# Optimization experiments

Hardware: AMD Instinct MI355X
Metric: run time of the kernel (lower is better)

The kernel has to match this reference:

```python
import jax, jax.numpy as jnp
import numpy as np

N, E, D, H, Z = 100000, 1600000, 128, 256, 64


def _gconv(x, src, dst, W, b, n):
    # DGL GraphConv, norm='both': D_in^{-1/2} A D_out^{-1/2} x W + b
    ones = jnp.ones(src.shape, x.dtype)
    deg_out = jnp.clip(jax.ops.segment_sum(ones, src, num_segments=n), 1.0)
    deg_in = jnp.clip(jax.ops.segment_sum(ones, dst, num_segments=n), 1.0)
    h = x * (deg_out ** -0.5)[:, None]          # scale by src out-degree
    agg = jax.ops.segment_sum(h[src], dst, num_segments=n)  # SpMM gather/scatter
    return (agg * (deg_in ** -0.5)[:, None]) @ W + b


def setup_inputs() -> dict:
    key = jax.random.key(0)
    ks = jax.random.split(key, 8)
    return {
        "features": jax.random.normal(ks[0], (N, D), jnp.float32),
        "src": jax.random.randint(ks[1], (E,), 0, N, jnp.int32),
        "dst": jax.random.randint(ks[2], (E,), 0, N, jnp.int32),
        "eps": jax.random.normal(ks[3], (N, Z), jnp.float32),
        "W1": jax.random.normal(ks[4], (D, H), jnp.float32) * (1.0 / np.sqrt(D)),
        "b1": jnp.zeros((H,), jnp.float32),
        "W2": jax.random.normal(ks[5], (H, 2 * Z), jnp.float32) * (1.0 / np.sqrt(H)),
        "b2": jnp.zeros((2 * Z,), jnp.float32),
        "W3": jax.random.normal(ks[6], (Z, D), jnp.float32) * (1.0 / np.sqrt(Z)),
        "b3": jnp.zeros((D,), jnp.float32),
    }


def reference(features, src, dst, eps, W1, b1, W2, b2, W3, b3):
    n = features.shape[0]
    h = jax.nn.relu(_gconv(features, src, dst, W1, b1, n))
    mean_logvar = _gconv(h, src, dst, W2, b2, n)
    mean, log_var = jnp.split(mean_logvar, 2, axis=1)
    z = eps * jnp.exp(0.5 * log_var) + mean  # reparameterization
    recon = _gconv(z, src, dst, W3, b3, n)
    return recon, mean, log_var
```

## Files before the change

### kernel.cpp

```cpp
#include <hip/hip_runtime.h>
#include <math.h>


#define MAXD 64
#define FBSH 8
#define EPT  16

typedef short short8 __attribute__((ext_vector_type(8)));
typedef float f32x4 __attribute__((ext_vector_type(4)));

__device__ __forceinline__ unsigned short f2bf(float f) {
  union { float f; unsigned u; } c; c.f = f;
  unsigned r = c.u + 0x7FFF + ((c.u >> 16) & 1);
  return (unsigned short)(r >> 16);
}
__device__ __forceinline__ float bf2f(unsigned short b) {
  return __builtin_bit_cast(float, (unsigned)b << 16);
}

__global__ __launch_bounds__(256) void k_bucket2(const int* __restrict__ src,
    const int* __restrict__ dst, int* __restrict__ bcd, int* __restrict__ bcs,
    int* __restrict__ bktd, unsigned char* __restrict__ srec,
    int E, int NFB, int cap2) {
  extern __shared__ int sh[];
  int* lcd = sh;
  int* lbd = sh + NFB;
  int* lcs = sh + 2 * NFB;
  int* lbs = sh + 3 * NFB;
  int tid = threadIdx.x;
  for (int i = tid; i < 4 * NFB; i += 256) sh[i] = 0;
  __syncthreads();
  int e0 = blockIdx.x * (256 * EPT);
  #pragma unroll 4
  for (int j = 0; j < EPT; j++) {
    int e = e0 + j * 256 + tid;
    if (e < E) {
      int d = dst[e]; atomicAdd(&lcd[d >> FBSH], 1);
      int s = src[e]; atomicAdd(&lcs[s >> FBSH], 1);
    }
  }
  __syncthreads();
  for (int fb = tid; fb < NFB; fb += 256) {
    int c = lcd[fb];
    if (c) lbd[fb] = atomicAdd(&bcd[fb], c);
    int cs = lcs[fb];
    if (cs) lbs[fb] = atomicAdd(&bcs[fb], cs);
  }
  __syncthreads();
  #pragma unroll 4
  for (int j = 0; j < EPT; j++) {
    int e = e0 + j * 256 + tid;
    if (e < E) {
      int d = dst[e]; int s = src[e];
      int fbd = d >> FBSH;
      int od = atomicAdd(&lbd[fbd], 1);
      if (od < cap2) bktd[(size_t)fbd * cap2 + od] = ((d & 255) << 24) | s;
      int fbs = s >> FBSH;
      int os = atomicAdd(&lbs[fbs], 1);
      if (os < cap2) srec[(size_t)fbs * cap2 + os] = (unsigned char)(s & 255);
    }
  }
}

__global__ __launch_bounds__(256) void k_csr(const int* __restrict__ bktd,
    const int* __restrict__ bcd, int* __restrict__ cnt, int* __restrict__ ebuf,
    int N, int cap2) {
  __shared__ int lcnt[256];
  int fb = blockIdx.x;
  int tid = threadIdx.x;
  lcnt[tid] = 0;
  __syncthreads();
  int m = bcd[fb]; m = m < cap2 ? m : cap2;
  const int* rec = bktd + (size_t)fb * cap2;
  for (int i0 = tid * 4; i0 < m; i0 += 1024) {
    if (i0 + 4 <= m) {
      int4 r = *(const int4*)(rec + i0);
      int dl, s, p;
      dl = (unsigned)r.x >> 24; s = r.x & 0xFFFFFF;
      p = atomicAdd(&lcnt[dl], 1);
      if (p < MAXD) ebuf[((size_t)(fb << FBSH) + dl) * MAXD + p] = s;
      dl = (unsigned)r.y >> 24; s = r.y & 0xFFFFFF;
      p = atomicAdd(&lcnt[dl], 1);
      if (p < MAXD) ebuf[((size_t)(fb << FBSH) + dl) * MAXD + p] = s;
      dl = (unsigned)r.z >> 24; s = r.z & 0xFFFFFF;
      p = atomicAdd(&lcnt[dl], 1);
      if (p < MAXD) ebuf[((size_t)(fb << FBSH) + dl) * MAXD + p] = s;
      dl = (unsigned)r.w >> 24; s = r.w & 0xFFFFFF;
      p = atomicAdd(&lcnt[dl], 1);
      if (p < MAXD) ebuf[((size_t)(fb << FBSH) + dl) * MAXD + p] = s;
    } else {
      for (int k = i0; k < m; k++) {
        int r = rec[k];
        int dl = (unsigned)r >> 24; int s = r & 0xFFFFFF;
        int p = atomicAdd(&lcnt[dl], 1);
        if (p < MAXD) ebuf[((size_t)(fb << FBSH) + dl) * MAXD + p] = s;
      }
    }
  }
  __syncthreads();
  int node = (fb << FBSH) + tid;
  if (node < N) cnt[node] = lcnt[tid];
}

__global__ __launch_bounds__(256) void k_deg(const unsigned char* __restrict__ srec,
    const int* __restrict__ bcs, int* __restrict__ degout, int N, int cap2) {
  __shared__ int lh[256];
  int fb = blockIdx.x;
  int tid = threadIdx.x;
  lh[tid] = 0;
  __syncthreads();
  int m = bcs[fb]; m = m < cap2 ? m : cap2;
  const unsigned char* rec = srec + (size_t)fb * cap2;
  for (int i0 = tid * 4; i0 < m; i0 += 1024) {
    if (i0 + 4 <= m) {
      uchar4 r = *(const uchar4*)(rec + i0);
      atomicAdd(&lh[r.x], 1); atomicAdd(&lh[r.y], 1);
      atomicAdd(&lh[r.z], 1); atomicAdd(&lh[r.w], 1);
    } else {
      for (int k = i0; k < m; k++) atomicAdd(&lh[rec[k]], 1);
    }
  }
  __syncthreads();
  int node = (fb << FBSH) + tid;
  if (node < N) degout[node] = lh[tid];
}

__global__ __launch_bounds__(256) void k_scale(const int* __restrict__ degout,
    const int* __restrict__ cnt, float* __restrict__ sout,
    float* __restrict__ sin_, int N) {
  int i = blockIdx.x * 256 + threadIdx.x;
  if (i >= N) return;
  int dO = degout[i]; if (dO < 1) dO = 1;
  int dI = cnt[i];    if (dI < 1) dI = 1;
  sout[i] = rsqrtf((float)dO);
  sin_[i] = rsqrtf((float)dI);
}

__global__ __launch_bounds__(256) void k_cvt(const float* __restrict__ in,
    unsigned short* __restrict__ out, int n) {
  int i = (blockIdx.x * 256 + threadIdx.x) * 4;
  if (i >= n) return;
  float4 f = *(const float4*)(in + i);
  unsigned lo = (unsigned)f2bf(f.x) | ((unsigned)f2bf(f.y) << 16);
  unsigned hi = (unsigned)f2bf(f.z) | ((unsigned)f2bf(f.w) << 16);
  uint2 o; o.x = lo; o.y = hi;
  *(uint2*)(out + i) = o;
}

template <int K, int OC>
__global__ __launch_bounds__(256) void k_wrepack(const float* __restrict__ W,
    short* __restrict__ Wp) {
  constexpr int KC = K / 32;
  constexpr int TOT = (OC / 16) * KC * 64;
  int t = blockIdx.x * 256 + threadIdx.x;
  if (t >= TOT) return;
  int lane = t & 63;
  int kc = (t >> 6) % KC;
  int nt = t / (KC * 64);
  int n = nt * 16 + (lane & 15);
  int k0 = kc * 32 + ((lane >> 4) * 8);
  short8 v;
  #pragma unroll
  for (int j = 0; j < 8; j++) v[j] = (short)f2bf(W[(size_t)(k0 + j) * OC + n]);
  *(short8*)(Wp + (size_t)t * 8) = v;
}

template <int K, int OC, bool RELU, bool BIAS, bool OUTBF16>
__global__ __launch_bounds__(256) void k_gemm_mfma(
    const unsigned short* __restrict__ A, const short* __restrict__ Wp,
    const float* __restrict__ bias, void* __restrict__ Cout, int N) {
  constexpr int KC = K / 32;
  constexpr int NT = OC / 16;
  int lane = threadIdx.x & 63;
  int wv = threadIdx.x >> 6;
  int m0 = (blockIdx.x * 4 + wv) * 16;
  if (m0 >= N) return;
  int mrow = m0 + (lane & 15);
  if (mrow >= N) mrow = N - 1;
  int q = lane >> 4;
  short8 av[KC];
  #pragma unroll
  for (int kc = 0; kc < KC; kc++)
    av[kc] = *(const short8*)(A + (size_t)mrow * K + kc * 32 + q * 8);
  int col0 = lane & 15;
  int rbase = m0 + q * 4;
  #pragma unroll
  for (int nt = 0; nt < NT; nt++) {
    f32x4 acc = {0.f, 0.f, 0.f, 0.f};
    #pragma unroll
    for (int kc = 0; kc < KC; kc++) {
      short8 bv = *(const short8*)(Wp + ((size_t)(nt * KC + kc) * 64 + lane) * 8);
      acc = __builtin_amdgcn_mfma_f32_16x16x32_bf16(av[kc], bv, acc, 0, 0, 0);
    }
    int col = nt * 16 + col0;
    float bb = BIAS ? bias[col] : 0.f;
    #pragma unroll
    for (int r = 0; r < 4; r++) {
      int row = rbase + r;
      if (row < N) {
        float v = acc[r] + bb;
        if (RELU) v = fmaxf(v, 0.f);
        if (OUTBF16) ((unsigned short*)Cout)[(size_t)row * OC + col] = f2bf(v);
        else         ((float*)Cout)[(size_t)row * OC + col] = v;
      }
    }
  }
}

__global__ __launch_bounds__(256) void k_spmm128b(const unsigned short* __restrict__ x,
    const int* __restrict__ ebuf, const int* __restrict__ cnt,
    const float* __restrict__ sout, const float* __restrict__ sin_,
    unsigned short* __restrict__ out, int N) {
  int lane = threadIdx.x & 63;
  int v = blockIdx.x * 4 + (threadIdx.x >> 6);
  if (v >= N) return;
  v = __builtin_amdgcn_readfirstlane(v);
  int c = cnt[v]; c = c < MAXD ? c : MAXD;
  const int* el = ebuf + (size_t)v * MAXD;
  int u_l = 0; float w_l = 0.f;
  if (lane < c) { u_l = el[lane]; w_l = sout[u_l]; }
  float ax = 0.f, ay = 0.f;
  int i = 0;
  for (; i + 4 <= c; i += 4) {
    #pragma unroll
    for (int j = 0; j < 4; j++) {
      int u = __shfl(u_l, i + j);
      float w = __shfl(w_l, i + j);
      unsigned p = *(const unsigned*)(x + (size_t)u * 128 + lane * 2);
      float lo = __builtin_bit_cast(float, p << 16);
      float hi = __builtin_bit_cast(float, p & 0xFFFF0000u);
      ax = fmaf(w, lo, ax); ay = fmaf(w, hi, ay);
    }
  }
  for (; i < c; i++) {
    int u = __shfl(u_l, i);
    float w = __shfl(w_l, i);
    unsigned p = *(const unsigned*)(x + (size_t)u * 128 + lane * 2);
    float lo = __builtin_bit_cast(float, p << 16);
    float hi = __builtin_bit_cast(float, p & 0xFFFF0000u);
    ax = fmaf(w, lo, ax); ay = fmaf(w, hi, ay);
  }
  float sv = sin_[v];
  unsigned o = (unsigned)f2bf(sv * ax) | ((unsigned)f2bf(sv * ay) << 16);
  *(unsigned*)(out + (size_t)v * 128 + lane * 2) = o;
}

__global__ __launch_bounds__(256) void k_spmm2b(const unsigned short* __restrict__ hw,
    const int* __restrict__ ebuf, const int* __restrict__ cnt,
    const float* __restrict__ sout, const float* __restrict__ sin_,
    const float* __restrict__ b2, const float* __restrict__ eps,
    float* __restrict__ mean_out, float* __restrict__ logvar_out,
    unsigned short* __restrict__ z, int N) {
  int lane = threadIdx.x & 63;
  int v = blockIdx.x * 4 + (threadIdx.x >> 6);
  if (v >= N) return;
  v = __builtin_amdgcn_readfirstlane(v);
  int c = cnt[v]; c = c < MAXD ? c : MAXD;
  const int* el = ebuf + (size_t)v * MAXD;
  int u_l = 0; float w_l = 0.f;
  if (lane < c) { u_l = el[lane]; w_l = sout[u_l]; }
  float ax = 0.f, ay = 0.f;
  int i = 0;
  for (; i + 4 <= c; i += 4) {
    #pragma unroll
    for (int j = 0; j < 4; j++) {
      int u = __shfl(u_l, i + j);
      float w = __shfl(w_l, i + j);
      unsigned p = *(const unsigned*)(hw + (size_t)u * 128 + lane * 2);
      float lo = __builtin_bit_cast(float, p << 16);
      float hi = __builtin_bit_cast(float, p & 0xFFFF0000u);
      ax = fmaf(w, lo, ax); ay = fmaf(w, hi, ay);
    }
  }
  for (; i < c; i++) {
    int u = __shfl(u_l, i);
    float w = __shfl(w_l, i);
    unsigned p = *(const unsigned*)(hw + (size_t)u * 128 + lane * 2);
    float lo = __builtin_bit_cast(float, p << 16);
    float hi = __builtin_bit_cast(float, p & 0xFFFF0000u);
    ax = fmaf(w, lo, ax); ay = fmaf(w, hi, ay);
  }
  float sv = sin_[v];
  float2 bb = ((const float2*)b2)[lane];
  float mx = fmaf(sv, ax, bb.x);
  float my = fmaf(sv, ay, bb.y);
  if (lane < 32) ((float2*)mean_out)[(size_t)v * 32 + lane] = make_float2(mx, my);
  else           ((float2*)logvar_out)[(size_t)v * 32 + (lane - 32)] = make_float2(mx, my);
  float lx = __shfl(mx, (lane & 31) + 32);
  float ly = __shfl(my, (lane & 31) + 32);
  if (lane < 32) {
    float2 e2 = ((const float2*)eps)[(size_t)v * 32 + lane];
    float zx = fmaf(e2.x, expf(0.5f * lx), mx);
    float zy = fmaf(e2.y, expf(0.5f * ly), my);
    unsigned o = (unsigned)f2bf(zx) | ((unsigned)f2bf(zy) << 16);
    *(unsigned*)(z + (size_t)v * 64 + lane * 2) = o;
  }
}

__global__ __launch_bounds__(256) void k_spmm64b(const unsigned short* __restrict__ z,
    const int* __restrict__ ebuf, const int* __restrict__ cnt,
    const float* __restrict__ sout, const float* __restrict__ sin_,
    unsigned short* __restrict__ aggz, int N) {
  int lane = threadIdx.x & 63;
  int v = blockIdx.x * 4 + (threadIdx.x >> 6);
  if (v >= N) return;
  v = __builtin_amdgcn_readfirstlane(v);
  int c = cnt[v]; c = c < MAXD ? c : MAXD;
  const int* el = ebuf + (size_t)v * MAXD;
  int u_l = 0; float w_l = 0.f;
  if (lane < c) { u_l = el[lane]; w_l = sout[u_l]; }
  float a = 0.f;
  int i = 0;
  for (; i + 8 <= c; i += 8) {
    #pragma unroll
    for (int j = 0; j < 8; j++) {
      int u = __shfl(u_l, i + j);
      float w = __shfl(w_l, i + j);
      a = fmaf(w, bf2f(z[(size_t)u * 64 + lane]), a);
    }
  }
  for (; i < c; i++) {
    int u = __shfl(u_l, i);
    float w = __shfl(w_l, i);
    a = fmaf(w, bf2f(z[(size_t)u * 64 + lane]), a);
  }
  aggz[(size_t)v * 64 + lane] = f2bf(sin_[v] * a);
}

extern "C" void kernel_launch(void* const* d_in, const int* in_sizes, int n_in,
                              void* d_out, int out_size, void* d_ws, size_t ws_size,
                              hipStream_t stream) {
  const float* features = (const float*)d_in[0];
  const int*   src      = (const int*)d_in[1];
  const int*   dst      = (const int*)d_in[2];
  const float* eps      = (const float*)d_in[3];
  const float* W1       = (const float*)d_in[4];
  const float* b1       = (const float*)d_in[5];
  const float* W2       = (const float*)d_in[6];
  const float* b2       = (const float*)d_in[7];
  const float* W3       = (const float*)d_in[8];
  const float* b3       = (const float*)d_in[9];
  const int E = in_sizes[1];
  const int N = in_sizes[3] / 64;
  float* out = (float*)d_out;

  const int NFB = (N + 255) >> FBSH;
  const int cap2 = ((E / NFB) + 2048 + 255) & ~255;

  char* ws = (char*)d_ws;
  int* degout = (int*)ws;            ws += (size_t)N * 4;
  int* cnt    = (int*)ws;            ws += (size_t)N * 4;
  int* bcd    = (int*)ws;            ws += (size_t)NFB * 4;
  int* bcs    = (int*)ws;            ws += (size_t)NFB * 4;
  int* ebuf   = (int*)ws;            ws += (size_t)N * MAXD * 4;
  float* sout = (float*)ws;          ws += (size_t)N * 4;
  float* sin_ = (float*)ws;          ws += (size_t)N * 4;
  short* W1p  = (short*)ws;          ws += 128 * 256 * 2;
  short* W2p  = (short*)ws;          ws += 256 * 128 * 2;
  short* W3p  = (short*)ws;          ws += 64 * 128 * 2;
  char* R1    = ws;                  ws += (size_t)N * 256;
  char* R2    = ws;                  ws += (size_t)N * 256;

  unsigned short* xb    = (unsigned short*)R1;
  unsigned short* hwb   = (unsigned short*)R1;
  unsigned short* aggzb = (unsigned short*)R1;
  unsigned short* agg1b = (unsigned short*)R2;
  unsigned short* zb    = (unsigned short*)R2;
  int* bktd = (int*)R2;
  unsigned char* srec = (unsigned char*)(R2 + (size_t)NFB * cap2 * 4);

  unsigned short* h     = (unsigned short*)out;
  float* recon          = out;
  float* mean_out       = out + (size_t)N * 128;
  float* logvar_out     = out + (size_t)N * 192;

  hipMemsetAsync(degout, 0, (size_t)N * 8 + (size_t)NFB * 8, stream);

  const size_t shA = (size_t)4 * NFB * 4;
  k_bucket2<<<(E + 256 * EPT - 1) / (256 * EPT), 256, shA, stream>>>(
      src, dst, bcd, bcs, bktd, srec, E, NFB, cap2);
  k_csr<<<NFB, 256, 0, stream>>>(bktd, bcd, cnt, ebuf, N, cap2);
  k_deg<<<NFB, 256, 0, stream>>>(srec, bcs, degout, N, cap2);
  k_scale<<<(N + 255) / 256, 256, 0, stream>>>(degout, cnt, sout, sin_, N);
  k_cvt<<<((N * 128 / 4) + 255) / 256, 256, 0, stream>>>(features, xb, N * 128);
  k_wrepack<128, 256><<<16, 256, 0, stream>>>(W1, W1p);
  k_wrepack<256, 128><<<16, 256, 0, stream>>>(W2, W2p);
  k_wrepack<64, 128><<<4, 256, 0, stream>>>(W3, W3p);

  k_spmm128b<<<(N + 3) / 4, 256, 0, stream>>>(xb, ebuf, cnt, sout, sin_, agg1b, N);
  k_gemm_mfma<128, 256, true, true, true>
      <<<(N + 63) / 64, 256, 0, stream>>>(agg1b, W1p, b1, h, N);

  k_gemm_mfma<256, 128, false, false, true>
      <<<(N + 63) / 64, 256, 0, stream>>>(h, W2p, nullptr, hwb, N);
  k_spmm2b<<<(N + 3) / 4, 256, 0, stream>>>(hwb, ebuf, cnt, sout, sin_, b2, eps,
                                            mean_out, logvar_out, zb, N);

  k_spmm64b<<<(N + 3) / 4, 256, 0, stream>>>(zb, ebuf, cnt, sout, sin_, aggzb, N);
  k_gemm_mfma<64, 128, false, true, false>
      <<<(N + 63) / 64, 256, 0, stream>>>(aggzb, W3p, b3, recon, N);
}
```

Baseline: 541.2 us.

## Pre-scale rows by source-degree norm and vectorize SpMM gathers to 16-byte loads

```diff
diff --git a/kernel.cpp b/kernel.cpp
--- a/kernel.cpp
+++ b/kernel.cpp
@@ -63,8 +63,8 @@
 }
 
 __global__ __launch_bounds__(256) void k_csr(const int* __restrict__ bktd,
-    const int* __restrict__ bcd, int* __restrict__ cnt, int* __restrict__ ebuf,
-    int N, int cap2) {
+    const int* __restrict__ bcd, int* __restrict__ cnt, float* __restrict__ sin_,
+    int* __restrict__ ebuf, int N, int cap2) {
   __shared__ int lcnt[256];
   int fb = blockIdx.x;
   int tid = threadIdx.x;
@@ -99,11 +99,15 @@
   }
   __syncthreads();
   int node = (fb << FBSH) + tid;
-  if (node < N) cnt[node] = lcnt[tid];
+  if (node < N) {
+    int c = lcnt[tid];
+    cnt[node] = c;
+    sin_[node] = rsqrtf((float)(c < 1 ? 1 : c));
+  }
 }
 
 __global__ __launch_bounds__(256) void k_deg(const unsigned char* __restrict__ srec,
-    const int* __restrict__ bcs, int* __restrict__ degout, int N, int cap2) {
+    const int* __restrict__ bcs, float* __restrict__ sout, int N, int cap2) {
   __shared__ int lh[256];
   int fb = blockIdx.x;
   int tid = threadIdx.x;
@@ -122,27 +126,20 @@
   }
   __syncthreads();
   int node = (fb << FBSH) + tid;
-  if (node < N) degout[node] = lh[tid];
-}
-
-__global__ __launch_bounds__(256) void k_scale(const int* __restrict__ degout,
-    const int* __restrict__ cnt, float* __restrict__ sout,
-    float* __restrict__ sin_, int N) {
-  int i = blockIdx.x * 256 + threadIdx.x;
-  if (i >= N) return;
-  int dO = degout[i]; if (dO < 1) dO = 1;
-  int dI = cnt[i];    if (dI < 1) dI = 1;
-  sout[i] = rsqrtf((float)dO);
-  sin_[i] = rsqrtf((float)dI);
+  if (node < N) {
+    int d = lh[tid];
+    sout[node] = rsqrtf((float)(d < 1 ? 1 : d));
+  }
 }
 
 __global__ __launch_bounds__(256) void k_cvt(const float* __restrict__ in,
-    unsigned short* __restrict__ out, int n) {
+    const float* __restrict__ sout, unsigned short* __restrict__ out, int n) {
   int i = (blockIdx.x * 256 + threadIdx.x) * 4;
   if (i >= n) return;
+  float s = sout[i >> 7];
   float4 f = *(const float4*)(in + i);
-  unsigned lo = (unsigned)f2bf(f.x) | ((unsigned)f2bf(f.y) << 16);
-  unsigned hi = (unsigned)f2bf(f.z) | ((unsigned)f2bf(f.w) << 16);
+  unsigned lo = (unsigned)f2bf(s * f.x) | ((unsigned)f2bf(s * f.y) << 16);
+  unsigned hi = (unsigned)f2bf(s * f.z) | ((unsigned)f2bf(s * f.w) << 16);
   uint2 o; o.x = lo; o.y = hi;
   *(uint2*)(out + i) = o;
 }
@@ -165,10 +162,11 @@
   *(short8*)(Wp + (size_t)t * 8) = v;
 }
 
-template <int K, int OC, bool RELU, bool BIAS, bool OUTBF16>
+template <int K, int OC, bool RELU, bool BIAS, bool OUTBF16, bool SOUT>
 __global__ __launch_bounds__(256) void k_gemm_mfma(
     const unsigned short* __restrict__ A, const short* __restrict__ Wp,
-    const float* __restrict__ bias, void* __restrict__ Cout, int N) {
+    const float* __restrict__ bias, const float* __restrict__ srow,
+    void* __restrict__ Cout, int N) {
   constexpr int KC = K / 32;
   constexpr int NT = OC / 16;
   int lane = threadIdx.x & 63;
@@ -184,6 +182,14 @@
     av[kc] = *(const short8*)(A + (size_t)mrow * K + kc * 32 + q * 8);
   int col0 = lane & 15;
   int rbase = m0 + q * 4;
+  float sr[4];
+  if (SOUT) {
+    #pragma unroll
+    for (int r = 0; r < 4; r++) {
+      int row = rbase + r;
+      sr[r] = (row < N) ? srow[row] : 1.f;
+    }
+  }
   #pragma unroll
   for (int nt = 0; nt < NT; nt++) {
     f32x4 acc = {0.f, 0.f, 0.f, 0.f};
@@ -200,6 +206,7 @@
       if (row < N) {
         float v = acc[r] + bb;
         if (RELU) v = fmaxf(v, 0.f);
+        if (SOUT) v *= sr[r];
         if (OUTBF16) ((unsigned short*)Cout)[(size_t)row * OC + col] = f2bf(v);
         else         ((float*)Cout)[(size_t)row * OC + col] = v;
       }
@@ -207,45 +214,73 @@
   }
 }
 
-__global__ __launch_bounds__(256) void k_spmm128b(const unsigned short* __restrict__ x,
+__global__ __launch_bounds__(256) void k_spmm128v(const unsigned short* __restrict__ x,
     const int* __restrict__ ebuf, const int* __restrict__ cnt,
-    const float* __restrict__ sout, const float* __restrict__ sin_,
-    unsigned short* __restrict__ out, int N) {
+    const float* __restrict__ sin_, unsigned short* __restrict__ out, int N) {
   int lane = threadIdx.x & 63;
   int v = blockIdx.x * 4 + (threadIdx.x >> 6);
   if (v >= N) return;
   v = __builtin_amdgcn_readfirstlane(v);
   int c = cnt[v]; c = c < MAXD ? c : MAXD;
   const int* el = ebuf + (size_t)v * MAXD;
-  int u_l = 0; float w_l = 0.f;
-  if (lane < c) { u_l = el[lane]; w_l = sout[u_l]; }
-  float ax = 0.f, ay = 0.f;
+  int u_l = (lane < c) ? el[lane] : 0;
+  int q = lane >> 4;
+  int fo = (lane & 15) * 8;
+  float a[8] = {0, 0, 0, 0, 0, 0, 0, 0};
   int i = 0;
-  for (; i + 4 <= c; i += 4) {
-    #pragma unroll
-    for (int j = 0; j < 4; j++) {
-      int u = __shfl(u_l, i + j);
-      float w = __shfl(w_l, i + j);
-      unsigned p = *(const unsigned*)(x + (size_t)u * 128 + lane * 2);
-      float lo = __builtin_bit_cast(float, p << 16);
-      float hi = __builtin_bit_cast(float, p & 0xFFFF0000u);
-      ax = fmaf(w, lo, ax); ay = fmaf(w, hi, ay);
-    }
-  }
-  for (; i < c; i++) {
-    int u = __shfl(u_l, i);
-    float w = __shfl(w_l, i);
-    unsigned p = *(const unsigned*)(x + (size_t)u * 128 + lane * 2);
-    float lo = __builtin_bit_cast(float, p << 16);
-    float hi = __builtin_bit_cast(float, p & 0xFFFF0000u);
-    ax = fmaf(w, lo, ax); ay = fmaf(w, hi, ay);
-  }
-  float sv = sin_[v];
-  unsigned o = (unsigned)f2bf(sv * ax) | ((unsigned)f2bf(sv * ay) << 16);
-  *(unsigned*)(out + (size_t)v * 128 + lane * 2) = o;
-}
-
-__global__ __launch_bounds__(256) void k_spmm2b(const unsigned short* __restrict__ hw,
+  for (; i + 8 <= c; i += 8) {
+    int u0 = __shfl(u_l, i + q);
+    int u1 = __shfl(u_l, i + 4 + q);
+    uint4 p0 = *(const uint4*)(x + (size_t)u0 * 128 + fo);
+    uint4 p1 = *(const uint4*)(x + (size_t)u1 * 128 + fo);
+    a[0] += __builtin_bit_cast(float, p0.x << 16);
+    a[1] += __builtin_bit_cast(float, p0.x & 0xFFFF0000u);
+    a[2] += __builtin_bit_cast(float, p0.y << 16);
+    a[3] += __builtin_bit_cast(float, p0.y & 0xFFFF0000u);
+    a[4] += __builtin_bit_cast(float, p0.z << 16);
+    a[5] += __builtin_bit_cast(float, p0.z & 0xFFFF0000u);
+    a[6] += __builtin_bit_cast(float, p0.w << 16);
+    a[7] += __builtin_bit_cast(float, p0.w & 0xFFFF0000u);
+    a[0] += __builtin_bit_cast(float, p1.x << 16);
+    a[1] += __builtin_bit_cast(float, p1.x & 0xFFFF0000u);
+    a[2] += __builtin_bit_cast(float, p1.y << 16);
+    a[3] += __builtin_bit_cast(float, p1.y & 0xFFFF0000u);
+    a[4] += __builtin_bit_cast(float, p1.z << 16);
+    a[5] += __builtin_bit_cast(float, p1.z & 0xFFFF0000u);
+    a[6] += __builtin_bit_cast(float, p1.w << 16);
+    a[7] += __builtin_bit_cast(float, p1.w & 0xFFFF0000u);
+  }
+  for (; i < c; i += 4) {
+    int eidx = i + q;
+    int u = __shfl(u_l, eidx);
+    uint4 p = *(const uint4*)(x + (size_t)u * 128 + fo);
+    if (eidx >= c) { p.x = 0; p.y = 0; p.z = 0; p.w = 0; }
+    a[0] += __builtin_bit_cast(float, p.x << 16);
+    a[1] += __builtin_bit_cast(float, p.x & 0xFFFF0000u);
+    a[2] += __builtin_bit_cast(float, p.y << 16);
+    a[3] += __builtin_bit_cast(float, p.y & 0xFFFF0000u);
+    a[4] += __builtin_bit_cast(float, p.z << 16);
+    a[5] += __builtin_bit_cast(float, p.z & 0xFFFF0000u);
+    a[6] += __builtin_bit_cast(float, p.w << 16);
+    a[7] += __builtin_bit_cast(float, p.w & 0xFFFF0000u);
+  }
+  #pragma unroll
+  for (int j = 0; j < 8; j++) {
+    a[j] += __shfl_xor(a[j], 16);
+    a[j] += __shfl_xor(a[j], 32);
+  }
+  if (lane < 16) {
+    float sv = sin_[v];
+    uint4 o;
+    o.x = (unsigned)f2bf(sv * a[0]) | ((unsigned)f2bf(sv * a[1]) << 16);
+    o.y = (unsigned)f2bf(sv * a[2]) | ((unsigned)f2bf(sv * a[3]) << 16);
+    o.z = (unsigned)f2bf(sv * a[4]) | ((unsigned)f2bf(sv * a[5]) << 16);
+    o.w = (unsigned)f2bf(sv * a[6]) | ((unsigned)f2bf(sv * a[7]) << 16);
+    *(uint4*)(out + (size_t)v * 128 + fo) = o;
+  }
+}
+
+__global__ __launch_bounds__(256) void k_spmm2v(const unsigned short* __restrict__ hw,
     const int* __restrict__ ebuf, const int* __restrict__ cnt,
     const float* __restrict__ sout, const float* __restrict__ sin_,
     const float* __restrict__ b2, const float* __restrict__ eps,
@@ -257,74 +292,151 @@
   v = __builtin_amdgcn_readfirstlane(v);
   int c = cnt[v]; c = c < MAXD ? c : MAXD;
   const int* el = ebuf + (size_t)v * MAXD;
-  int u_l = 0; float w_l = 0.f;
-  if (lane < c) { u_l = el[lane]; w_l = sout[u_l]; }
-  float ax = 0.f, ay = 0.f;
+  int u_l = (lane < c) ? el[lane] : 0;
+  int q = lane >> 4;
+  int fo = (lane & 15) * 8;
+  float a[8] = {0, 0, 0, 0, 0, 0, 0, 0};
   int i = 0;
-  for (; i + 4 <= c; i += 4) {
-    #pragma unroll
-    for (int j = 0; j < 4; j++) {
-      int u = __shfl(u_l, i + j);
-      float w = __shfl(w_l, i + j);
-      unsigned p = *(const unsigned*)(hw + (size_t)u * 128 + lane * 2);
-      float lo = __builtin_bit_cast(float, p << 16);
-      float hi = __builtin_bit_cast(float, p & 0xFFFF0000u);
-      ax = fmaf(w, lo, ax); ay = fmaf(w, hi, ay);
-    }
-  }
-  for (; i < c; i++) {
-    int u = __shfl(u_l, i);
-    float w = __shfl(w_l, i);
-    unsigned p = *(const unsigned*)(hw + (size_t)u * 128 + lane * 2);
-    float lo = __builtin_bit_cast(float, p << 16);
-    float hi = __builtin_bit_cast(float, p & 0xFFFF0000u);
-    ax = fmaf(w, lo, ax); ay = fmaf(w, hi, ay);
+  for (; i + 8 <= c; i += 8) {
+    int u0 = __shfl(u_l, i + q);
+    int u1 = __shfl(u_l, i + 4 + q);
+    uint4 p0 = *(const uint4*)(hw + (size_t)u0 * 128 + fo);
+    uint4 p1 = *(const uint4*)(hw + (size_t)u1 * 128 + fo);
+    a[0] += __builtin_bit_cast(float, p0.x << 16);
+    a[1] += __builtin_bit_cast(float, p0.x & 0xFFFF0000u);
+    a[2] += __builtin_bit_cast(float, p0.y << 16);
+    a[3] += __builtin_bit_cast(float, p0.y & 0xFFFF0000u);
+    a[4] += __builtin_bit_cast(float, p0.z << 16);
+    a[5] += __builtin_bit_cast(float, p0.z & 0xFFFF0000u);
+    a[6] += __builtin_bit_cast(float, p0.w << 16);
+    a[7] += __builtin_bit_cast(float, p0.w & 0xFFFF0000u);
+    a[0] += __builtin_bit_cast(float, p1.x << 16);
+    a[1] += __builtin_bit_cast(float, p1.x & 0xFFFF0000u);
+    a[2] += __builtin_bit_cast(float, p1.y << 16);
+    a[3] += __builtin_bit_cast(float, p1.y & 0xFFFF0000u);
+    a[4] += __builtin_bit_cast(float, p1.z << 16);
+    a[5] += __builtin_bit_cast(float, p1.z & 0xFFFF0000u);
+    a[6] += __builtin_bit_cast(float, p1.w << 16);
+    a[7] += __builtin_bit_cast(float, p1.w & 0xFFFF0000u);
+  }
+  for (; i < c; i += 4) {
+    int eidx = i + q;
+    int u = __shfl(u_l, eidx);
+    uint4 p = *(const uint4*)(hw + (size_t)u * 128 + fo);
+    if (eidx >= c) { p.x = 0; p.y = 0; p.z = 0; p.w = 0; }
+    a[0] += __builtin_bit_cast(float, p.x << 16);
+    a[1] += __builtin_bit_cast(float, p.x & 0xFFFF0000u);
+    a[2] += __builtin_bit_cast(float, p.y << 16);
+    a[3] += __builtin_bit_cast(float, p.y & 0xFFFF0000u);
+    a[4] += __builtin_bit_cast(float, p.z << 16);
+    a[5] += __builtin_bit_cast(float, p.z & 0xFFFF0000u);
+    a[6] += __builtin_bit_cast(float, p.w << 16);
+    a[7] += __builtin_bit_cast(float, p.w & 0xFFFF0000u);
+  }
+  #pragma unroll
+  for (int j = 0; j < 8; j++) {
+    a[j] += __shfl_xor(a[j], 16);
+    a[j] += __shfl_xor(a[j], 32);
   }
   float sv = sin_[v];
-  float2 bb = ((const float2*)b2)[lane];
-  float mx = fmaf(sv, ax, bb.x);
-  float my = fmaf(sv, ay, bb.y);
-  if (lane < 32) ((float2*)mean_out)[(size_t)v * 32 + lane] = make_float2(mx, my);
-  else           ((float2*)logvar_out)[(size_t)v * 32 + (lane - 32)] = make_float2(mx, my);
-  float lx = __shfl(mx, (lane & 31) + 32);
-  float ly = __shfl(my, (lane & 31) + 32);
-  if (lane < 32) {
-    float2 e2 = ((const float2*)eps)[(size_t)v * 32 + lane];
-    float zx = fmaf(e2.x, expf(0.5f * lx), mx);
-    float zy = fmaf(e2.y, expf(0.5f * ly), my);
-    unsigned o = (unsigned)f2bf(zx) | ((unsigned)f2bf(zy) << 16);
-    *(unsigned*)(z + (size_t)v * 64 + lane * 2) = o;
-  }
-}
-
-__global__ __launch_bounds__(256) void k_spmm64b(const unsigned short* __restrict__ z,
+  float4 blo = *(const float4*)(b2 + fo);
+  float4 bhi = *(const float4*)(b2 + fo + 4);
+  float m[8];
+  m[0] = fmaf(sv, a[0], blo.x); m[1] = fmaf(sv, a[1], blo.y);
+  m[2] = fmaf(sv, a[2], blo.z); m[3] = fmaf(sv, a[3], blo.w);
+  m[4] = fmaf(sv, a[4], bhi.x); m[5] = fmaf(sv, a[5], bhi.y);
+  m[6] = fmaf(sv, a[6], bhi.z); m[7] = fmaf(sv, a[7], bhi.w);
+  float lv[8];
+  #pragma unroll
+  for (int j = 0; j < 8; j++) lv[j] = __shfl_xor(m[j], 8);
+  int k = lane & 15;
+  if (lane < 16) {
+    if (k < 8) {
+      *(float4*)(mean_out + (size_t)v * 64 + k * 8) =
+          make_float4(m[0], m[1], m[2], m[3]);
+      *(float4*)(mean_out + (size_t)v * 64 + k * 8 + 4) =
+          make_float4(m[4], m[5], m[6], m[7]);
+      float so = sout[v];
+      float4 e0 = *(const float4*)(eps + (size_t)v * 64 + k * 8);
+      float4 e1 = *(const float4*)(eps + (size_t)v * 64 + k * 8 + 4);
+      float z0 = so * fmaf(e0.x, expf(0.5f * lv[0]), m[0]);
+      float z1 = so * fmaf(e0.y, expf(0.5f * lv[1]), m[1]);
+      float z2 = so * fmaf(e0.z, expf(0.5f * lv[2]), m[2]);
+      float z3 = so * fmaf(e0.w, expf(0.5f * lv[3]), m[3]);
+      float z4 = so * fmaf(e1.x, expf(0.5f * lv[4]), m[4]);
+      float z5 = so * fmaf(e1.y, expf(0.5f * lv[5]), m[5]);
+      float z6 = so * fmaf(e1.z, expf(0.5f * lv[6]), m[6]);
+      float z7 = so * fmaf(e1.w, expf(0.5f * lv[7]), m[7]);
+      uint4 o;
+      o.x = (unsigned)f2bf(z0) | ((unsigned)f2bf(z1) << 16);
+      o.y = (unsigned)f2bf(z2) | ((unsigned)f2bf(z3) << 16);
+      o.z = (unsigned)f2bf(z4) | ((unsigned)f2bf(z5) << 16);
+      o.w = (unsigned)f2bf(z6) | ((unsigned)f2bf(z7) << 16);
+      *(uint4*)(z + (size_t)v * 64 + k * 8) = o;
+    } else {
+      *(float4*)(logvar_out + (size_t)v * 64 + (k - 8) * 8) =
+          make_float4(m[0], m[1], m[2], m[3]);
+      *(float4*)(logvar_out + (size_t)v * 64 + (k - 8) * 8 + 4) =
+          make_float4(m[4], m[5], m[6], m[7]);
+    }
+  }
+}
+
+__global__ __launch_bounds__(256) void k_spmm64v(const unsigned short* __restrict__ z,
     const int* __restrict__ ebuf, const int* __restrict__ cnt,
-    const float* __restrict__ sout, const float* __restrict__ sin_,
-    unsigned short* __restrict__ aggz, int N) {
+    const float* __restrict__ sin_, unsigned short* __restrict__ aggz, int N) {
   int lane = threadIdx.x & 63;
   int v = blockIdx.x * 4 + (threadIdx.x >> 6);
   if (v >= N) return;
   v = __builtin_amdgcn_readfirstlane(v);
   int c = cnt[v]; c = c < MAXD ? c : MAXD;
   const int* el = ebuf + (size_t)v * MAXD;
-  int u_l = 0; float w_l = 0.f;
-  if (lane < c) { u_l = el[lane]; w_l = sout[u_l]; }
-  float a = 0.f;
+  int u_l = (lane < c) ? el[lane] : 0;
+  int o8 = lane >> 3;
+  int fo = (lane & 7) * 8;
+  float a[8] = {0, 0, 0, 0, 0, 0, 0, 0};
   int i = 0;
   for (; i + 8 <= c; i += 8) {
-    #pragma unroll
-    for (int j = 0; j < 8; j++) {
-      int u = __shfl(u_l, i + j);
-      float w = __shfl(w_l, i + j);
-      a = fmaf(w, bf2f(z[(size_t)u * 64 + lane]), a);
-    }
-  }
-  for (; i < c; i++) {
-    int u = __shfl(u_l, i);
-    float w = __shfl(w_l, i);
-    a = fmaf(w, bf2f(z[(size_t)u * 64 + lane]), a);
-  }
-  aggz[(size_t)v * 64 + lane] = f2bf(sin_[v] * a);
+    int u = __shfl(u_l, i + o8);
+    uint4 p = *(const uint4*)(z + (size_t)u * 64 + fo);
+    a[0] += __builtin_bit_cast(float, p.x << 16);
+    a[1] += __builtin_bit_cast(float, p.x & 0xFFFF0000u);
+    a[2] += __builtin_bit_cast(float, p.y << 16);
+    a[3] += __builtin_bit_cast(float, p.y & 0xFFFF0000u);
+    a[4] += __builtin_bit_cast(float, p.z << 16);
+    a[5] += __builtin_bit_cast(float, p.z & 0xFFFF0000u);
+    a[6] += __builtin_bit_cast(float, p.w << 16);
+    a[7] += __builtin_bit_cast(float, p.w & 0xFFFF0000u);
+  }
+  if (i < c) {
+    int eidx = i + o8;
+    int u = __shfl(u_l, eidx);
+    uint4 p = *(const uint4*)(z + (size_t)u * 64 + fo);
+    if (eidx >= c) { p.x = 0; p.y = 0; p.z = 0; p.w = 0; }
+    a[0] += __builtin_bit_cast(float, p.x << 16);
+    a[1] += __builtin_bit_cast(float, p.x & 0xFFFF0000u);
+    a[2] += __builtin_bit_cast(float, p.y << 16);
+    a[3] += __builtin_bit_cast(float, p.y & 0xFFFF0000u);
+    a[4] += __builtin_bit_cast(float, p.z << 16);
+    a[5] += __builtin_bit_cast(float, p.z & 0xFFFF0000u);
+    a[6] += __builtin_bit_cast(float, p.w << 16);
+    a[7] += __builtin_bit_cast(float, p.w & 0xFFFF0000u);
+  }
+  #pragma unroll
+  for (int j = 0; j < 8; j++) {
+    a[j] += __shfl_xor(a[j], 8);
+    a[j] += __shfl_xor(a[j], 16);
+    a[j] += __shfl_xor(a[j], 32);
+  }
+  if (lane < 8) {
+    float sv = sin_[v];
+    uint4 o;
+    o.x = (unsigned)f2bf(sv * a[0]) | ((unsigned)f2bf(sv * a[1]) << 16);
+    o.y = (unsigned)f2bf(sv * a[2]) | ((unsigned)f2bf(sv * a[3]) << 16);
+    o.z = (unsigned)f2bf(sv * a[4]) | ((unsigned)f2bf(sv * a[5]) << 16);
+    o.w = (unsigned)f2bf(sv * a[6]) | ((unsigned)f2bf(sv * a[7]) << 16);
+    *(uint4*)(aggz + (size_t)v * 64 + fo) = o;
+  }
 }
 
 extern "C" void kernel_launch(void* const* d_in, const int* in_sizes, int n_in,
@@ -348,7 +460,6 @@
   const int cap2 = ((E / NFB) + 2048 + 255) & ~255;
 
   char* ws = (char*)d_ws;
-  int* degout = (int*)ws;            ws += (size_t)N * 4;
   int* cnt    = (int*)ws;            ws += (size_t)N * 4;
   int* bcd    = (int*)ws;            ws += (size_t)NFB * 4;
   int* bcs    = (int*)ws;            ws += (size_t)NFB * 4;
@@ -374,29 +485,28 @@
   float* mean_out       = out + (size_t)N * 128;
   float* logvar_out     = out + (size_t)N * 192;
 
-  hipMemsetAsync(degout, 0, (size_t)N * 8 + (size_t)NFB * 8, stream);
+  hipMemsetAsync(bcd, 0, (size_t)NFB * 8, stream);
 
   const size_t shA = (size_t)4 * NFB * 4;
   k_bucket2<<<(E + 256 * EPT - 1) / (256 * EPT), 256, shA, stream>>>(
       src, dst, bcd, bcs, bktd, srec, E, NFB, cap2);
-  k_csr<<<NFB, 256, 0, stream>>>(bktd, bcd, cnt, ebuf, N, cap2);
-  k_deg<<<NFB, 256, 0, stream>>>(srec, bcs, degout, N, cap2);
-  k_scale<<<(N + 255) / 256, 256, 0, stream>>>(degout, cnt, sout, sin_, N);
-  k_cvt<<<((N * 128 / 4) + 255) / 256, 256, 0, stream>>>(features, xb, N * 128);
+  k_csr<<<NFB, 256, 0, stream>>>(bktd, bcd, cnt, sin_, ebuf, N, cap2);
+  k_deg<<<NFB, 256, 0, stream>>>(srec, bcs, sout, N, cap2);
+  k_cvt<<<((N * 128 / 4) + 255) / 256, 256, 0, stream>>>(features, sout, xb, N * 128);
   k_wrepack<128, 256><<<16, 256, 0, stream>>>(W1, W1p);
   k_wrepack<256, 128><<<16, 256, 0, stream>>>(W2, W2p);
   k_wrepack<64, 128><<<4, 256, 0, stream>>>(W3, W3p);
 
-  k_spmm128b<<<(N + 3) / 4, 256, 0, stream>>>(xb, ebuf, cnt, sout, sin_, agg1b, N);
-  k_gemm_mfma<128, 256, true, true, true>
-      <<<(N + 63) / 64, 256, 0, stream>>>(agg1b, W1p, b1, h, N);
-
-  k_gemm_mfma<256, 128, false, false, true>
-      <<<(N + 63) / 64, 256, 0, stream>>>(h, W2p, nullptr, hwb, N);
-  k_spmm2b<<<(N + 3) / 4, 256, 0, stream>>>(hwb, ebuf, cnt, sout, sin_, b2, eps,
+  k_spmm128v<<<(N + 3) / 4, 256, 0, stream>>>(xb, ebuf, cnt, sin_, agg1b, N);
+  k_gemm_mfma<128, 256, true, true, true, true>
+      <<<(N + 63) / 64, 256, 0, stream>>>(agg1b, W1p, b1, sout, h, N);
+
+  k_gemm_mfma<256, 128, false, false, true, false>
+      <<<(N + 63) / 64, 256, 0, stream>>>(h, W2p, nullptr, nullptr, hwb, N);
+  k_spmm2v<<<(N + 3) / 4, 256, 0, stream>>>(hwb, ebuf, cnt, sout, sin_, b2, eps,
                                             mean_out, logvar_out, zb, N);
 
-  k_spmm64b<<<(N + 3) / 4, 256, 0, stream>>>(zb, ebuf, cnt, sout, sin_, aggzb, N);
-  k_gemm_mfma<64, 128, false, true, false>
-      <<<(N + 63) / 64, 256, 0, stream>>>(aggzb, W3p, b3, recon, N);
-}
+  k_spmm64v<<<(N + 3) / 4, 256, 0, stream>>>(zb, ebuf, cnt, sin_, aggzb, N);
+  k_gemm_mfma<64, 128, false, true, false, false>
+      <<<(N + 63) / 64, 256, 0, stream>>>(aggzb, W3p, b3, nullptr, recon, N);
+}
```

Result: faster. 526.6 us (-2.7%).
